# Kernel tuning notes

Hardware: AMD Instinct MI355X
Metric: run time of the kernel (lower is better)

Reference implementation:

```python
import jax, jax.numpy as jnp
import numpy as np

TEMPERATURE = 0.07
EPS = 1e-12  # F.normalize eps


def _construct_labels(visual_ids, anchor_idx):
    # Faithful vectorization of the original order-dependent double loop:
    # for i < B-1: final write to labels[i] comes from pair (i, B-1)
    #   -> 1 iff ids[i]==anchor_id and ids[B-1]==anchor_id, else 0
    # for i == B-1: final write comes from pair (B-2, B-1)
    #   -> 1 iff ids[B-1]==anchor_id and ids[B-2]==anchor_id, else 0
    B = visual_ids.shape[0]
    anchor_id = visual_ids[anchor_idx]
    same = visual_ids == anchor_id  # [B] bool
    labels = jnp.where(same & same[B - 1], 1, 0).astype(jnp.int32)
    labels = labels.at[B - 1].set((same[B - 1] & same[B - 2]).astype(jnp.int32))
    return labels


def setup_inputs() -> dict:
    key = jax.random.key(0)
    k1, k2 = jax.random.split(key)
    visual_feat = jax.random.normal(k1, (8192, 512), dtype=jnp.float32)
    visual_ids = jax.random.randint(k2, (8192,), 0, 1024, dtype=jnp.int64 if jax.config.jax_enable_x64 else jnp.int32)
    anchor_idx = 3
    return {"visual_feat": visual_feat, "visual_ids": visual_ids, "anchor_idx": anchor_idx}


def reference(visual_feat, visual_ids, anchor_idx):
    # L2 normalize rows (F.normalize: x / max(||x||, eps))
    norm = jnp.sqrt(jnp.sum(visual_feat * visual_feat, axis=1, keepdims=True))
    f = visual_feat / jnp.maximum(norm, EPS)
    sim = jnp.matmul(f, f.T) / TEMPERATURE  # [B, B]
    labels = _construct_labels(visual_ids, anchor_idx)  # [B] int in {0,1}
    logp = jax.nn.log_softmax(sim, axis=-1)  # [B, B]
    picked = jnp.take_along_axis(logp, labels[:, None], axis=1)[:, 0]
    loss = -jnp.mean(picked)
    return loss
```

## Files before the change

### kernel.cpp

```cpp
#include <hip/hip_runtime.h>


typedef int i32x8 __attribute__((ext_vector_type(8)));
typedef float f32x4 __attribute__((ext_vector_type(4)));

#define B_N 8192
#define D_K 512
#define ROWB 512
#define INVT 14.285714285714286f
#define SCALE_LOG2 20.609929155556622f

#if defined(__has_builtin) && __has_builtin(__builtin_amdgcn_exp2f)
#define FAST_EXP2(x) __builtin_amdgcn_exp2f(x)
#else
#define FAST_EXP2(x) exp2f(x)
#endif

union FragU {
  int4 h[2];
  i32x8 v;
};

static __device__ __forceinline__ void load16_to_lds(const void* g, void* l) {
  __builtin_amdgcn_global_load_lds(
      (const __attribute__((address_space(1))) unsigned int*)g,
      (__attribute__((address_space(3))) unsigned int*)l, 16, 0, 0);
}

__global__ __launch_bounds__(256)
void norm_kernel(const float* __restrict__ x,
                 unsigned char* __restrict__ fQ,
                 float* __restrict__ Z) {
  const int row = blockIdx.x * 4 + (threadIdx.x >> 6);
  const int lane = threadIdx.x & 63;
  const float4* xr = (const float4*)(x + (size_t)row * D_K);
  float4 a = xr[2 * lane];
  float4 b = xr[2 * lane + 1];
  float s = a.x * a.x + a.y * a.y + a.z * a.z + a.w * a.w +
            b.x * b.x + b.y * b.y + b.z * b.z + b.w * b.w;
#pragma unroll
  for (int off = 1; off < 64; off <<= 1) s += __shfl_xor(s, off);
  const float inv = 1.0f / fmaxf(sqrtf(s), 1e-12f);
  int lo = 0, hi = 0;
  lo = __builtin_amdgcn_cvt_pk_fp8_f32(a.x * inv, a.y * inv, lo, false);
  lo = __builtin_amdgcn_cvt_pk_fp8_f32(a.z * inv, a.w * inv, lo, true);
  hi = __builtin_amdgcn_cvt_pk_fp8_f32(b.x * inv, b.y * inv, hi, false);
  hi = __builtin_amdgcn_cvt_pk_fp8_f32(b.z * inv, b.w * inv, hi, true);
  int2 p; p.x = lo; p.y = hi;
  ((int2*)(fQ + (size_t)row * ROWB))[lane] = p;
  if (lane == 0) Z[row] = 0.0f;
}

__global__ __launch_bounds__(256, 2)
void sim_kernel(const unsigned char* __restrict__ fQ,
                float* __restrict__ Z, float* __restrict__ T01,
                float* __restrict__ D) {
  __shared__ unsigned char ldsA[4][128 * 128];
  __shared__ unsigned char ldsB[128 * 128];

  const int tid = threadIdx.x;
  const int lane = tid & 63;
  const int w = tid >> 6;
  const int wm = w & 1;
  const int wn = w >> 1;
  const int bx = blockIdx.x, by = blockIdx.y;
  const int I0 = bx * 128;
  const int Jbase = by * 1024;

  const int srow = lane >> 3;
  const int sb = lane & 7;
  const int su = sb ^ srow;
  const int sg = 2 * (su & 3) + (su >> 2);
  const size_t sOff = (size_t)srow * ROWB + sg * 16;

  const int fr = lane & 15;
  const int q = lane >> 4;
  const int swz = fr & 7;

  const int raRow = (wm * 64 + fr) * 128;
  const unsigned char* rbBase = ldsB + (wn * 64 + fr) * 128;
  const int off0 = (q ^ swz) * 16;
  const int off1 = ((q + 4) ^ swz) * 16;

#pragma unroll
  for (int kk = 0; kk < 4; ++kk) {
    const unsigned char* gA = fQ + (size_t)(I0 + w * 32) * ROWB + kk * 128 + sOff;
    unsigned char* lA = ldsA[kk] + (w * 32) * 128;
#pragma unroll
    for (int rr = 0; rr < 32; rr += 8)
      load16_to_lds(gA + (size_t)rr * ROWB, lA + rr * 128);
  }

  float Zp[4][4];
#pragma unroll
  for (int m = 0; m < 4; ++m)
#pragma unroll
    for (int r = 0; r < 4; ++r) Zp[m][r] = 0.0f;

#pragma unroll 1
  for (int jt = 0; jt < 8; ++jt) {
    const int J0 = Jbase + jt * 128;
    f32x4 acc[4][4];
#pragma unroll
    for (int m = 0; m < 4; ++m)
#pragma unroll
      for (int n = 0; n < 4; ++n) acc[m][n] = (f32x4){0.f, 0.f, 0.f, 0.f};

#pragma unroll 1
    for (int kk = 0; kk < 4; ++kk) {
      const int k0 = kk * 128;
      {
        const unsigned char* gB = fQ + (size_t)(J0 + w * 32) * ROWB + k0 + sOff;
        unsigned char* lB = ldsB + (w * 32) * 128;
#pragma unroll
        for (int rr = 0; rr < 32; rr += 8)
          load16_to_lds(gB + (size_t)rr * ROWB, lB + rr * 128);
      }
      __syncthreads();

      const unsigned char* raBase = ldsA[kk] + raRow;
      i32x8 bv[4];
#pragma unroll
      for (int n = 0; n < 4; ++n) {
        const unsigned char* rb = rbBase + n * 16 * 128;
        FragU u;
        u.h[0] = *(const int4*)(rb + off0);
        u.h[1] = *(const int4*)(rb + off1);
        bv[n] = u.v;
      }
#pragma unroll
      for (int mh = 0; mh < 2; ++mh) {
        i32x8 av[2];
#pragma unroll
        for (int m = 0; m < 2; ++m) {
          const unsigned char* ra = raBase + (mh * 2 + m) * 16 * 128;
          FragU u;
          u.h[0] = *(const int4*)(ra + off0);
          u.h[1] = *(const int4*)(ra + off1);
          av[m] = u.v;
        }
#pragma unroll
        for (int m = 0; m < 2; ++m)
#pragma unroll
          for (int n = 0; n < 4; ++n)
            acc[mh * 2 + m][n] = __builtin_amdgcn_mfma_scale_f32_16x16x128_f8f6f4(
                av[m], bv[n], acc[mh * 2 + m][n], 0, 0, 0, 127, 0, 127);
      }
      __syncthreads();
    }

    if (by == 0 && jt == 0 && wn == 0 && fr < 2) {
#pragma unroll
      for (int m = 0; m < 4; ++m)
#pragma unroll
        for (int r = 0; r < 4; ++r) {
          const int row = I0 + wm * 64 + m * 16 + q * 4 + r;
          T01[row * 2 + fr] = acc[m][0][r] * INVT;
        }
    }

    if (by == (bx >> 3) && jt == (bx & 7)) {
#pragma unroll
      for (int m = 0; m < 4; ++m)
#pragma unroll
        for (int n = 0; n < 4; ++n) {
          const int col = J0 + wn * 64 + n * 16 + fr;
#pragma unroll
          for (int r = 0; r < 4; ++r) {
            const int row = I0 + wm * 64 + m * 16 + q * 4 + r;
            if (row == col) D[row] = acc[m][n][r];
          }
        }
    }

#pragma unroll
    for (int m = 0; m < 4; ++m)
#pragma unroll
      for (int n = 0; n < 4; ++n)
#pragma unroll
        for (int r = 0; r < 4; ++r)
          Zp[m][r] += FAST_EXP2((acc[m][n][r] - 1.0f) * SCALE_LOG2);
  }

#pragma unroll
  for (int m = 0; m < 4; ++m)
#pragma unroll
    for (int r = 0; r < 4; ++r) {
      float v = Zp[m][r];
      v += __shfl_xor(v, 1);
      v += __shfl_xor(v, 2);
      v += __shfl_xor(v, 4);
      v += __shfl_xor(v, 8);
      if (fr == 0) atomicAdd(&Z[I0 + wm * 64 + m * 16 + q * 4 + r], v);
    }
}

__global__ __launch_bounds__(1024)
void finalize_kernel(const float* __restrict__ Z,
                     const float* __restrict__ T01,
                     const float* __restrict__ D,
                     const int* __restrict__ ids,
                     const int* __restrict__ anchor,
                     float* __restrict__ out) {
  __shared__ float red[1024];
  const int t = threadIdx.x;
  const int anchor_id = ids[anchor[0]];
  const int sameLast = (ids[B_N - 1] == anchor_id);
  const int samePrev = (ids[B_N - 2] == anchor_id);
  int i[8], id[8];
  float z[8], d[8], t0[8], t1[8];
#pragma unroll
  for (int u = 0; u < 8; ++u) {
    i[u] = u * 1024 + t;
    z[u] = Z[i[u]];
    d[u] = D[i[u]];
    t0[u] = T01[i[u] * 2 + 0];
    t1[u] = T01[i[u] * 2 + 1];
    id[u] = ids[i[u]];
  }
  float sum = 0.0f;
#pragma unroll
  for (int u = 0; u < 8; ++u) {
    const int same_i = (id[u] == anchor_id);
    const int lab =
        (i[u] < B_N - 1) ? (same_i & sameLast) : (sameLast & samePrev);
    const float tt = lab ? t1[u] : t0[u];
    const float Zc = z[u] - FAST_EXP2((d[u] - 1.0f) * SCALE_LOG2) + 1.0f;
    sum += tt - (INVT + logf(Zc));
  }
  red[t] = sum;
  __syncthreads();
  for (int off = 512; off > 0; off >>= 1) {
    if (t < off) red[t] += red[t + off];
    __syncthreads();
  }
  if (t == 0) out[0] = -red[0] / (float)B_N;
}

extern "C" void kernel_launch(void* const* d_in, const int* in_sizes, int n_in,
                              void* d_out, int out_size, void* d_ws, size_t ws_size,
                              hipStream_t stream) {
  const float* x = (const float*)d_in[0];
  const int* ids = (const int*)d_in[1];
  const int* anchor = (const int*)d_in[2];
  float* out = (float*)d_out;

  unsigned char* fQ = (unsigned char*)d_ws;
  float* Z = (float*)((char*)d_ws + (size_t)B_N * ROWB);
  float* T01 = Z + B_N;
  float* D = T01 + 2 * B_N;

  norm_kernel<<<B_N / 4, 256, 0, stream>>>(x, fQ, Z);
  sim_kernel<<<dim3(64, 8), 256, 0, stream>>>(fQ, Z, T01, D);
  finalize_kernel<<<1, 1024, 0, stream>>>(Z, T01, D, ids, anchor, out);
}
```

Before: 113.0 us.

## Exploit Gram matrix symmetry: compute upper-triangle tiles, add column sums to Z

The similarity matrix f·fᵀ is symmetric, so each block now computes only tiles with J >= I and reuses each off-diagonal tile twice. Row exp-sums feed Z[I] as before, and column exp-sums are reduced across the wave and atomically added to Z[J]. The grid is remapped to 32x16 with mirrored row pairing (I and 63-I) so per-block work stays balanced, and T01 is now read from row 0 columns instead of columns 0/1. This roughly halves MFMA work in exchange for extra shuffles and many more global atomics.

Measured after the change: 104.4 us. 1.08x faster.

```diff
diff --git a/kernel.cpp b/kernel.cpp
--- a/kernel.cpp
+++ b/kernel.cpp
@@ -64,8 +64,11 @@
   const int wm = w & 1;
   const int wn = w >> 1;
   const int bx = blockIdx.x, by = blockIdx.y;
-  const int I0 = bx * 128;
-  const int Jbase = by * 1024;
+  const int b = by & 7;
+  const int I = (by < 8) ? bx : (63 - bx);
+  const int Jfirst = I + ((b - I) & 7);
+  if (Jfirst > 63) return;
+  const int I0 = I * 128;
 
   const int srow = lane >> 3;
   const int sb = lane & 7;
@@ -98,8 +101,8 @@
     for (int r = 0; r < 4; ++r) Zp[m][r] = 0.0f;
 
 #pragma unroll 1
-  for (int jt = 0; jt < 8; ++jt) {
-    const int J0 = Jbase + jt * 128;
+  for (int J = Jfirst; J < 64; J += 8) {
+    const int J0 = J * 128;
     f32x4 acc[4][4];
 #pragma unroll
     for (int m = 0; m < 4; ++m)
@@ -149,17 +152,18 @@
       __syncthreads();
     }
 
-    if (by == 0 && jt == 0 && wn == 0 && fr < 2) {
-#pragma unroll
-      for (int m = 0; m < 4; ++m)
-#pragma unroll
-        for (int r = 0; r < 4; ++r) {
-          const int row = I0 + wm * 64 + m * 16 + q * 4 + r;
-          T01[row * 2 + fr] = acc[m][0][r] * INVT;
-        }
-    }
-
-    if (by == (bx >> 3) && jt == (bx & 7)) {
+    if (I == 0 && wm == 0) {
+      if (q == 0) {
+#pragma unroll
+        for (int n = 0; n < 4; ++n) {
+          const int col = J0 + wn * 64 + n * 16 + fr;
+          T01[col * 2 + 0] = acc[0][n][0] * INVT;
+          T01[col * 2 + 1] = acc[0][n][1] * INVT;
+        }
+      }
+    }
+
+    if (J == I) {
 #pragma unroll
       for (int m = 0; m < 4; ++m)
 #pragma unroll
@@ -173,13 +177,24 @@
         }
     }
 
-#pragma unroll
-    for (int m = 0; m < 4; ++m)
-#pragma unroll
-      for (int n = 0; n < 4; ++n)
-#pragma unroll
-        for (int r = 0; r < 4; ++r)
-          Zp[m][r] += FAST_EXP2((acc[m][n][r] - 1.0f) * SCALE_LOG2);
+    const bool offd = (J != I);
+#pragma unroll
+    for (int n = 0; n < 4; ++n) {
+      float cs = 0.0f;
+#pragma unroll
+      for (int m = 0; m < 4; ++m)
+#pragma unroll
+        for (int r = 0; r < 4; ++r) {
+          const float e = FAST_EXP2((acc[m][n][r] - 1.0f) * SCALE_LOG2);
+          Zp[m][r] += e;
+          cs += e;
+        }
+      if (offd) {
+        cs += __shfl_xor(cs, 16);
+        cs += __shfl_xor(cs, 32);
+        if (q == 0) atomicAdd(&Z[J0 + wn * 64 + n * 16 + fr], cs);
+      }
+    }
   }
 
 #pragma unroll
@@ -251,6 +266,6 @@
   float* D = T01 + 2 * B_N;
 
   norm_kernel<<<B_N / 4, 256, 0, stream>>>(x, fQ, Z);
-  sim_kernel<<<dim3(64, 8), 256, 0, stream>>>(fQ, Z, T01, D);
+  sim_kernel<<<dim3(32, 16), 256, 0, stream>>>(fQ, Z, T01, D);
   finalize_kernel<<<1, 1024, 0, stream>>>(Z, T01, D, ids, anchor, out);
 }
```
